# Performance work log

Measured on AMD Instinct MI355X. Metric: run time of the kernel, lower is better.

## Reference

```python
import jax, jax.numpy as jnp
import numpy as np

B, T, P, E = 4, 16, 256, 768
H, D = 12, 64          # num_heads, kq_size; H*D == E
DFF = 3072
SCALE = D ** (-0.5)
EPS = 1e-5


def _ln(x, g, b):
    m = jnp.mean(x, axis=-1, keepdims=True)
    v = jnp.mean((x - m) ** 2, axis=-1, keepdims=True)
    return (x - m) / jnp.sqrt(v + EPS) * g + b


def setup_inputs() -> dict:
    key = jax.random.key(0)
    ks = jax.random.split(key, 16)
    std = 0.02
    d = {"x": jax.random.normal(ks[0], (B, T, P, E), jnp.float32)}
    # spatial attention params (weights stored as (in, out))
    d["sq_w"] = jax.random.normal(ks[1], (E, H * D), jnp.float32) * std
    d["sk_w"] = jax.random.normal(ks[2], (E, H * D), jnp.float32) * std
    d["sv_w"] = jax.random.normal(ks[3], (E, H * D), jnp.float32) * std
    d["so_w"] = jax.random.normal(ks[4], (H * D, E), jnp.float32) * std
    d["sq_b"] = jnp.zeros((H * D,), jnp.float32)
    d["sk_b"] = jnp.zeros((H * D,), jnp.float32)
    d["sv_b"] = jnp.zeros((H * D,), jnp.float32)
    d["so_b"] = jnp.zeros((E,), jnp.float32)
    d["sg"] = jnp.ones((E,), jnp.float32)
    d["sb"] = jnp.zeros((E,), jnp.float32)
    # temporal attention params
    d["tq_w"] = jax.random.normal(ks[5], (E, H * D), jnp.float32) * std
    d["tk_w"] = jax.random.normal(ks[6], (E, H * D), jnp.float32) * std
    d["tv_w"] = jax.random.normal(ks[7], (E, H * D), jnp.float32) * std
    d["to_w"] = jax.random.normal(ks[8], (H * D, E), jnp.float32) * std
    d["tq_b"] = jnp.zeros((H * D,), jnp.float32)
    d["tk_b"] = jnp.zeros((H * D,), jnp.float32)
    d["tv_b"] = jnp.zeros((H * D,), jnp.float32)
    d["to_b"] = jnp.zeros((E,), jnp.float32)
    d["tg"] = jnp.ones((E,), jnp.float32)
    d["tb"] = jnp.zeros((E,), jnp.float32)
    # FFN + final layernorm
    d["w1"] = jax.random.normal(ks[9], (E, DFF), jnp.float32) * std
    d["b1"] = jnp.zeros((DFF,), jnp.float32)
    d["w2"] = jax.random.normal(ks[10], (DFF, E), jnp.float32) * std
    d["b2"] = jnp.zeros((E,), jnp.float32)
    d["g"] = jnp.ones((E,), jnp.float32)
    d["bb"] = jnp.zeros((E,), jnp.float32)
    return d


def reference(x, sq_w, sq_b, sk_w, sk_b, sv_w, sv_b, so_w, so_b, sg, sb,
              tq_w, tq_b, tk_w, tk_b, tv_w, tv_b, to_w, to_b, tg, tb,
              w1, b1, w2, b2, g, bb):
    b, t, p, e = x.shape

    # ---- Spatial layer: attention over patches P within each frame ----
    q = (x @ sq_w + sq_b).reshape(b, t, p, H, D)
    k = (x @ sk_w + sk_b).reshape(b, t, p, H, D)
    v = (x @ sv_w + sv_b).reshape(b, t, p, H, D)
    attn = jnp.einsum('btphd,btqhd->bthpq', q, k) * SCALE
    attn = jax.nn.softmax(attn, axis=-1)
    out = jnp.einsum('bthpq,btqhd->btphd', attn, v).reshape(b, t, p, H * D)
    out = out @ so_w + so_b
    x = _ln(x + out, sg, sb)

    # ---- Temporal layer: causal attention over frames T per patch ----
    q = (x @ tq_w + tq_b).reshape(b, t, p, H, D)
    k = (x @ tk_w + tk_b).reshape(b, t, p, H, D)
    v = (x @ tv_w + tv_b).reshape(b, t, p, H, D)
    attn = jnp.einsum('btphd,bsphd->bphts', q, k) * SCALE
    causal = jnp.where(jnp.arange(t)[:, None] >= jnp.arange(t)[None, :],
                       jnp.float32(0), -jnp.inf).astype(x.dtype)  # (T, T)
    attn = attn + causal
    attn = jax.nn.softmax(attn, axis=-1)
    out = jnp.einsum('bphts,bsphd->btphd', attn, v).reshape(b, t, p, H * D)
    out = out @ to_w + to_b
    x = _ln(x + out, tg, tb)

    # ---- Feed forward + final layernorm ----
    ff = jax.nn.gelu(x @ w1 + b1, approximate=False) @ w2 + b2
    x = _ln(x + ff, g, bb)
    return x
```

## Files before the change

kernel.cpp:

```cpp
#include <hip/hip_runtime.h>
#include <math.h>

constexpr int cB   = 4;
constexpr int cT   = 16;
constexpr int cP   = 256;
constexpr int cE   = 768;
constexpr int cH   = 12;
constexpr int cD   = 64;
constexpr int cDFF = 3072;
constexpr int NTOK = cB * cT * cP;
constexpr float cSCALE = 0.125f;
constexpr float cEPS = 1e-5f;

typedef __attribute__((ext_vector_type(8))) short short8;
typedef __attribute__((ext_vector_type(4))) float f32x4;
typedef __attribute__((ext_vector_type(8))) unsigned short u16x8;
typedef __attribute__((ext_vector_type(4))) unsigned short u16x4;

#define AS1 __attribute__((address_space(1)))
#define AS3 __attribute__((address_space(3)))

__device__ inline float b2f(unsigned short u) {
    union { unsigned int i; float f; } c; c.i = ((unsigned int)u) << 16; return c.f;
}
__device__ inline unsigned short f2b(float f) {
    union { float f; unsigned int i; } c; c.f = f;
    unsigned int i = c.i;
    unsigned int r = i + 0x7FFFu + ((i >> 16) & 1u);
    return (unsigned short)(r >> 16);
}

__device__ inline void gload16(const unsigned short* g, short* l) {
    __builtin_amdgcn_global_load_lds((AS1 const void*)g, (AS3 void*)l, 16, 0, 0);
}

__device__ inline void stage_half(const unsigned short* Xg, int K,
                                  short* ldsbase, int w, int l) {
    #pragma unroll
    for (int j = 0; j < 2; ++j) {
        const int r = w * 16 + j * 8 + (l >> 3);
        const int sl = l & 7;
        gload16(Xg + (size_t)r * K + ((sl ^ (r & 7)) << 3),
                ldsbase + r * 64 + (sl << 3));
    }
}

template<int OUTB, int ACT, int SPLIT3>
__global__ __launch_bounds__(512, 2) void gemm256_kernel(
    const unsigned short* __restrict__ A,
    const unsigned short* __restrict__ BT,
    const float* __restrict__ bias0, const float* __restrict__ bias1,
    const float* __restrict__ bias2,
    void* __restrict__ C0, void* __restrict__ C1, void* __restrict__ C2,
    int M, int N, int K, int nbn)
{
    __shared__ short As[2 * 256 * 64];
    __shared__ short Bs[2 * 256 * 64];

    const int tid = threadIdx.x;
    const int w = tid >> 6, l = tid & 63;
    const int l15 = l & 15, l16 = l >> 4;
    const int wm = w >> 2, wn = w & 3;

    const int nwg = gridDim.x;
    const int wg = (blockIdx.x & 7) * (nwg >> 3) + (blockIdx.x >> 3);
    const int bm = wg / nbn, bn = wg % nbn;
    const int m0 = bm * 256, n0 = bn * 256;

    const unsigned short* pA0 = A + (size_t)m0 * K;
    const unsigned short* pA1 = A + (size_t)(m0 + 128) * K;
    const unsigned short* pB0 = BT + (size_t)n0 * K;
    const unsigned short* pB1 = BT + (size_t)(n0 + 128) * K;

    f32x4 acc[8][4];
    #pragma unroll
    for (int i = 0; i < 8; ++i)
        #pragma unroll
        for (int j = 0; j < 4; ++j)
            #pragma unroll
            for (int r = 0; r < 4; ++r) acc[i][j][r] = 0.f;

    stage_half(pA0, K, As, w, l);
    stage_half(pA1, K, As + 8192, w, l);
    stage_half(pB0, K, Bs, w, l);
    stage_half(pB1, K, Bs + 8192, w, l);
    asm volatile("s_waitcnt vmcnt(0)" ::: "memory");
    __builtin_amdgcn_s_barrier();

    short8 bF[4][2];
    const int niter = K >> 7;
    int k0 = 0;
    for (int it = 0; it < niter; ++it) {
        const int kb = k0 + 64;
        const int kc = (k0 + 128 < K) ? (k0 + 128) : 0;
        #pragma unroll
        for (int p = 0; p < 8; ++p) {
            const int c = p >> 2;
            const int q = p & 3;

            short8 aF[2][2];
            if (q == 0) {
                #pragma unroll
                for (int nf = 0; nf < 4; ++nf) {
                    const int rb = wn * 64 + nf * 16 + l15;
                    const char* pb = (const char*)Bs + c * 32768 + rb * 128;
                    const int sw = (rb & 7) << 4;
                    bF[nf][0] = *(const short8*)(pb + ((l16 * 16) ^ sw));
                    bF[nf][1] = *(const short8*)(pb + ((64 + l16 * 16) ^ sw));
                }
            }
            #pragma unroll
            for (int mm = 0; mm < 2; ++mm) {
                const int ra = wm * 128 + (q * 2 + mm) * 16 + l15;
                const char* pa = (const char*)As + c * 32768 + ra * 128;
                const int sw = (ra & 7) << 4;
                aF[mm][0] = *(const short8*)(pa + ((l16 * 16) ^ sw));
                aF[mm][1] = *(const short8*)(pa + ((64 + l16 * 16) ^ sw));
            }

            {
                const int koff = (p < 4) ? kb : kc;
                short* dst = ((q < 2) ? As : Bs) + ((c ^ 1) * 16384) + ((q & 1) * 8192);
                const unsigned short* src =
                    (q == 0 ? pA0 : q == 1 ? pA1 : q == 2 ? pB0 : pB1) + koff;
                stage_half(src, K, dst, w, l);
            }

            __builtin_amdgcn_s_barrier();
            asm volatile("s_waitcnt lgkmcnt(0)" ::: "memory");
            __builtin_amdgcn_sched_barrier(0);
            __builtin_amdgcn_s_setprio(1);
            #pragma unroll
            for (int kk = 0; kk < 2; ++kk)
                #pragma unroll
                for (int nf = 0; nf < 4; ++nf)
                    #pragma unroll
                    for (int mm = 0; mm < 2; ++mm)
                        acc[q * 2 + mm][nf] = __builtin_amdgcn_mfma_f32_16x16x32_bf16(
                            aF[mm][kk], bF[nf][kk], acc[q * 2 + mm][nf], 0, 0, 0);
            __builtin_amdgcn_s_setprio(0);
            __builtin_amdgcn_sched_barrier(0);
            if (q == 3)
                asm volatile("s_waitcnt vmcnt(0)" ::: "memory");
            __builtin_amdgcn_s_barrier();
        }
        k0 += 128;
    }

    #pragma unroll
    for (int mf = 0; mf < 8; ++mf) {
        #pragma unroll
        for (int nf = 0; nf < 4; ++nf) {
            const int ng = n0 + wn * 64 + nf * 16 + l15;
            int nl = ng;
            const float* bp = bias0;
            void* Cp = C0;
            int Nout = N;
            if (SPLIT3) {
                const int which = ng / 768;
                nl = ng - which * 768;
                bp = (which == 0) ? bias0 : (which == 1) ? bias1 : bias2;
                Cp = (which == 0) ? C0 : (which == 1) ? C1 : C2;
                Nout = 768;
            }
            const float bs = bp[nl];
            #pragma unroll
            for (int r = 0; r < 4; ++r) {
                const int row = m0 + wm * 128 + mf * 16 + l16 * 4 + r;
                float v = acc[mf][nf][r] + bs;
                if (ACT) v = 0.5f * v * (1.f + erff(v * 0.70710678118654752f));
                if (OUTB) ((unsigned short*)Cp)[(size_t)row * Nout + nl] = f2b(v);
                else      ((float*)Cp)[(size_t)row * Nout + nl] = v;
            }
        }
    }
}

__global__ __launch_bounds__(256) void transpose_cast_kernel(
    const float* __restrict__ W, unsigned short* __restrict__ WT,
    int K, int N)
{
    __shared__ float t[32][33];
    const int k0 = blockIdx.y * 32;
    const int n0 = blockIdx.x * 32;
    const int tx = threadIdx.x & 31;
    const int ty4 = (threadIdx.x >> 5) << 2;
    #pragma unroll
    for (int i = 0; i < 4; ++i)
        t[ty4 + i][tx] = W[(size_t)(k0 + ty4 + i) * N + n0 + tx];
    __syncthreads();
    #pragma unroll
    for (int i = 0; i < 4; ++i)
        WT[(size_t)(n0 + ty4 + i) * K + k0 + tx] = f2b(t[tx][ty4 + i]);
}

struct TP8 { const float* src[8]; unsigned short* dst[8]; };
__global__ __launch_bounds__(256) void transpose_cast8_kernel(TP8 p)
{
    __shared__ float t[32][33];
    const int z = blockIdx.z;
    const float* W = p.src[z];
    unsigned short* WT = p.dst[z];
    const int k0 = blockIdx.y * 32;
    const int n0 = blockIdx.x * 32;
    const int tx = threadIdx.x & 31;
    const int ty4 = (threadIdx.x >> 5) << 2;
    #pragma unroll
    for (int i = 0; i < 4; ++i)
        t[ty4 + i][tx] = W[(size_t)(k0 + ty4 + i) * cE + n0 + tx];
    __syncthreads();
    #pragma unroll
    for (int i = 0; i < 4; ++i)
        WT[(size_t)(n0 + ty4 + i) * cE + k0 + tx] = f2b(t[tx][ty4 + i]);
}

__global__ __launch_bounds__(256) void cast_bf16_kernel(
    const float* __restrict__ in, unsigned short* __restrict__ out, int n4)
{
    for (int i = blockIdx.x * blockDim.x + threadIdx.x; i < n4;
         i += gridDim.x * blockDim.x) {
        float4 v = ((const float4*)in)[i];
        u16x4 o;
        o[0] = f2b(v.x); o[1] = f2b(v.y); o[2] = f2b(v.z); o[3] = f2b(v.w);
        *(u16x4*)(out + (size_t)i * 4) = o;
    }
}

__global__ __launch_bounds__(256) void residual_ln_kernel(
    const float* __restrict__ X, const float* __restrict__ R,
    const float* __restrict__ gamma, const float* __restrict__ beta,
    float* __restrict__ out, unsigned short* __restrict__ outb)
{
    const int row = blockIdx.x;
    const size_t off = (size_t)row * cE;
    const int tid = threadIdx.x;

    float v[3];
    float s = 0.f, ss = 0.f;
    #pragma unroll
    for (int i = 0; i < 3; ++i) {
        const int e = tid + i * 256;
        const float t = X[off + e] + R[off + e];
        v[i] = t; s += t; ss += t * t;
    }
    #pragma unroll
    for (int o = 32; o > 0; o >>= 1) {
        s  += __shfl_down(s, o);
        ss += __shfl_down(ss, o);
    }
    __shared__ float rs[4], rss[4];
    const int wid = tid >> 6;
    if ((tid & 63) == 0) { rs[wid] = s; rss[wid] = ss; }
    __syncthreads();
    s  = rs[0] + rs[1] + rs[2] + rs[3];
    ss = rss[0] + rss[1] + rss[2] + rss[3];

    const float mean = s * (1.f / cE);
    const float var  = ss * (1.f / cE) - mean * mean;
    const float inv  = rsqrtf(var + cEPS);
    #pragma unroll
    for (int i = 0; i < 3; ++i) {
        const int e = tid + i * 256;
        const float r = (v[i] - mean) * inv * gamma[e] + beta[e];
        out[off + e] = r;
        if (outb) outb[off + e] = f2b(r);
    }
}

__global__ __launch_bounds__(256) void spatial_attn_mfma_kernel(
    const unsigned short* __restrict__ Q, const unsigned short* __restrict__ K,
    const unsigned short* __restrict__ V, unsigned short* __restrict__ O)
{
    __shared__ short Ks[64 * 64];
    __shared__ short Vt[64 * 64];
    __shared__ short Ps[4][64 * 64];

    const int bid = blockIdx.x;
    const int h  = bid % cH;
    const int bt = bid / cH;
    const size_t base = (size_t)bt * cP * cE + h * cD;

    const int tid = threadIdx.x;
    const int w = tid >> 6, l = tid & 63;
    const int l15 = l & 15, l16 = l >> 4;

    short8 qf[4][2];
    #pragma unroll
    for (int mf = 0; mf < 4; ++mf)
        #pragma unroll
        for (int kf = 0; kf < 2; ++kf)
            qf[mf][kf] = *(const short8*)(
                Q + base + (size_t)(w * 64 + mf * 16 + l15) * cE + kf * 32 + l16 * 8);

    f32x4 o[4][4];
    float mrun[4][4], lrun[4][4];
    #pragma unroll
    for (int mf = 0; mf < 4; ++mf)
        #pragma unroll
        for (int j = 0; j < 4; ++j) {
            #pragma unroll
            for (int r = 0; r < 4; ++r) o[mf][j][r] = 0.f;
            mrun[mf][j] = -INFINITY; lrun[mf][j] = 0.f;
        }

    const int krow = w * 8 + (l >> 3);
    const int kc16 = l & 7;
    const int vj  = tid & 31;
    const int vd0 = (tid >> 5) * 8;

    for (int c0 = 0; c0 < cP; c0 += 64) {
        __syncthreads();
        #pragma unroll
        for (int p = 0; p < 2; ++p) {
            const int row = p * 32 + krow;
            gload16(K + base + (size_t)(c0 + row) * cE + ((kc16 ^ (row & 7)) << 3),
                    Ks + row * 64 + kc16 * 8);
        }
        #pragma unroll
        for (int p = 0; p < 2; ++p) {
            const int j = p * 32 + vj;
            short8 vv = *(const short8*)(V + base + (size_t)(c0 + j) * cE + vd0);
            char* vb = (char*)Vt;
            #pragma unroll
            for (int e = 0; e < 8; ++e) {
                const int row = vd0 + e;
                *(short*)(vb + row * 128 + ((2 * j) ^ ((row & 7) << 4))) = vv[e];
            }
        }
        __syncthreads();

        f32x4 s[4][4];
        #pragma unroll
        for (int mf = 0; mf < 4; ++mf)
            #pragma unroll
            for (int nf = 0; nf < 4; ++nf)
                #pragma unroll
                for (int r = 0; r < 4; ++r) s[mf][nf][r] = 0.f;

        #pragma unroll
        for (int nf = 0; nf < 4; ++nf) {
            const int row = nf * 16 + l15;
            const char* kb = (const char*)Ks + row * 128;
            const int sw = (row & 7) << 4;
            short8 k0 = *(const short8*)(kb + ((l16 * 16) ^ sw));
            short8 k1 = *(const short8*)(kb + ((64 + l16 * 16) ^ sw));
            #pragma unroll
            for (int mf = 0; mf < 4; ++mf) {
                s[mf][nf] = __builtin_amdgcn_mfma_f32_16x16x32_bf16(qf[mf][0], k0, s[mf][nf], 0, 0, 0);
                s[mf][nf] = __builtin_amdgcn_mfma_f32_16x16x32_bf16(qf[mf][1], k1, s[mf][nf], 0, 0, 0);
            }
        }

        #pragma unroll
        for (int mf = 0; mf < 4; ++mf)
            #pragma unroll
            for (int nf = 0; nf < 4; ++nf)
                #pragma unroll
                for (int r = 0; r < 4; ++r) s[mf][nf][r] *= cSCALE;

        #pragma unroll
        for (int mf = 0; mf < 4; ++mf) {
            #pragma unroll
            for (int r = 0; r < 4; ++r) {
                float rv = fmaxf(fmaxf(s[mf][0][r], s[mf][1][r]),
                                 fmaxf(s[mf][2][r], s[mf][3][r]));
                rv = fmaxf(rv, __shfl_xor(rv, 1));
                rv = fmaxf(rv, __shfl_xor(rv, 2));
                rv = fmaxf(rv, __shfl_xor(rv, 4));
                rv = fmaxf(rv, __shfl_xor(rv, 8));
                const float mn = fmaxf(mrun[mf][r], rv);
                const float al = __expf(mrun[mf][r] - mn);
                mrun[mf][r] = mn;
                float ps = 0.f;
                #pragma unroll
                for (int nf = 0; nf < 4; ++nf) {
                    const float pe = __expf(s[mf][nf][r] - mn);
                    s[mf][nf][r] = pe;
                    ps += pe;
                }
                ps += __shfl_xor(ps, 1);
                ps += __shfl_xor(ps, 2);
                ps += __shfl_xor(ps, 4);
                ps += __shfl_xor(ps, 8);
                lrun[mf][r] = lrun[mf][r] * al + ps;
                #pragma unroll
                for (int df = 0; df < 4; ++df) o[mf][df][r] *= al;
            }
        }

        char* pw = (char*)&Ps[w][0];
        #pragma unroll
        for (int mf = 0; mf < 4; ++mf)
            #pragma unroll
            for (int nf = 0; nf < 4; ++nf)
                #pragma unroll
                for (int r = 0; r < 4; ++r) {
                    const int row = mf * 16 + l16 * 4 + r;
                    *(short*)(pw + row * 128 + (((nf * 16 + l15) * 2) ^ ((row & 7) << 4))) =
                        (short)f2b(s[mf][nf][r]);
                }

        short8 pa[4][2];
        #pragma unroll
        for (int mf = 0; mf < 4; ++mf) {
            const int prow = mf * 16 + l15;
            const char* pb = (const char*)&Ps[w][0] + prow * 128;
            const int sw = (prow & 7) << 4;
            pa[mf][0] = *(const short8*)(pb + ((l16 * 16) ^ sw));
            pa[mf][1] = *(const short8*)(pb + ((64 + l16 * 16) ^ sw));
        }
        #pragma unroll
        for (int df = 0; df < 4; ++df) {
            const int vrow = df * 16 + l15;
            const char* vbb = (const char*)Vt + vrow * 128;
            const int sw = (vrow & 7) << 4;
            short8 v0 = *(const short8*)(vbb + ((l16 * 16) ^ sw));
            short8 v1 = *(const short8*)(vbb + ((64 + l16 * 16) ^ sw));
            #pragma unroll
            for (int mf = 0; mf < 4; ++mf) {
                o[mf][df] = __builtin_amdgcn_mfma_f32_16x16x32_bf16(pa[mf][0], v0, o[mf][df], 0, 0, 0);
                o[mf][df] = __builtin_amdgcn_mfma_f32_16x16x32_bf16(pa[mf][1], v1, o[mf][df], 0, 0, 0);
            }
        }
    }

    #pragma unroll
    for (int mf = 0; mf < 4; ++mf)
        #pragma unroll
        for (int r = 0; r < 4; ++r) {
            const float inv = 1.f / lrun[mf][r];
            const size_t rowoff = base + (size_t)(w * 64 + mf * 16 + l16 * 4 + r) * cE;
            #pragma unroll
            for (int df = 0; df < 4; ++df)
                O[rowoff + df * 16 + l15] = f2b(o[mf][df][r] * inv);
        }
}

__global__ __launch_bounds__(128) void temporal_attn_kernel(
    const unsigned short* __restrict__ Q, const unsigned short* __restrict__ Kb,
    const unsigned short* __restrict__ V, unsigned short* __restrict__ O)
{
    const int bid = blockIdx.x;
    const int hg  = bid & 1;
    const int bp  = bid >> 1;
    const int p   = bp % cP;
    const int b   = bp / cP;

    __shared__ float Ks[cT][6][cD + 1];
    __shared__ float Vs[cT][6][cD + 1];

    const size_t framestride = (size_t)cP * cE;
    const size_t base0 = ((size_t)(b * cT) * cP + p) * cE + hg * 384;

    for (int li = threadIdx.x; li < cT * 384; li += 128) {
        const int s = li / 384;
        const int r = li % 384;
        const size_t src = base0 + (size_t)s * framestride + r;
        Ks[s][r / 64][r & 63] = b2f(Kb[src]);
        Vs[s][r / 64][r & 63] = b2f(V[src]);
    }
    __syncthreads();
    if (threadIdx.x >= 96) return;

    const int hh = threadIdx.x >> 4;
    const int t  = threadIdx.x & 15;
    const size_t qoff = ((size_t)(b * cT + t) * cP + p) * cE + hg * 384 + hh * cD;

    float q[cD];
    #pragma unroll
    for (int d = 0; d < cD; d += 8) {
        short8 f = *(const short8*)(Q + qoff + d);
        #pragma unroll
        for (int j = 0; j < 8; ++j) q[d + j] = b2f((unsigned short)f[j]);
    }

    float sc[cT];
    float mx = -INFINITY;
    #pragma unroll
    for (int s = 0; s < cT; ++s) {
        float acc = 0.f;
        #pragma unroll
        for (int d = 0; d < cD; ++d) acc = fmaf(q[d], Ks[s][hh][d], acc);
        sc[s] = (s <= t) ? acc * cSCALE : -INFINITY;
        mx = fmaxf(mx, sc[s]);
    }
    float l = 0.f;
    #pragma unroll
    for (int s = 0; s < cT; ++s) {
        const float e_ = __expf(sc[s] - mx);
        sc[s] = e_;
        l += e_;
    }
    float o[cD];
    #pragma unroll
    for (int d = 0; d < cD; ++d) o[d] = 0.f;
    #pragma unroll
    for (int s = 0; s < cT; ++s) {
        const float pj = sc[s];
        #pragma unroll
        for (int d = 0; d < cD; ++d) o[d] = fmaf(pj, Vs[s][hh][d], o[d]);
    }
    const float invl = 1.f / l;
    unsigned short* op = O + qoff;
    #pragma unroll
    for (int d = 0; d < cD; d += 8) {
        u16x8 f;
        #pragma unroll
        for (int j = 0; j < 8; ++j) f[j] = f2b(o[d + j] * invl);
        *(u16x8*)(op + d) = f;
    }
}

extern "C" void kernel_launch(void* const* d_in, const int* in_sizes, int n_in,
                              void* d_out, int out_size, void* d_ws, size_t ws_size,
                              hipStream_t stream)
{
    const float* x    = (const float*)d_in[0];
    const float* sq_w = (const float*)d_in[1];
    const float* sk_w = (const float*)d_in[2];
    const float* sv_w = (const float*)d_in[3];
    const float* so_w = (const float*)d_in[4];
    const float* sq_b = (const float*)d_in[5];
    const float* sk_b = (const float*)d_in[6];
    const float* sv_b = (const float*)d_in[7];
    const float* so_b = (const float*)d_in[8];
    const float* sg   = (const float*)d_in[9];
    const float* sb   = (const float*)d_in[10];
    const float* tq_w = (const float*)d_in[11];
    const float* tk_w = (const float*)d_in[12];
    const float* tv_w = (const float*)d_in[13];
    const float* to_w = (const float*)d_in[14];
    const float* tq_b = (const float*)d_in[15];
    const float* tk_b = (const float*)d_in[16];
    const float* tv_b = (const float*)d_in[17];
    const float* to_b = (const float*)d_in[18];
    const float* tg   = (const float*)d_in[19];
    const float* tb   = (const float*)d_in[20];
    const float* w1   = (const float*)d_in[21];
    const float* b1   = (const float*)d_in[22];
    const float* w2   = (const float*)d_in[23];
    const float* b2   = (const float*)d_in[24];
    const float* g    = (const float*)d_in[25];
    const float* bb   = (const float*)d_in[26];

    const size_t NE = (size_t)NTOK * cE;
    const size_t EE = (size_t)cE * cE;

    float* W0 = (float*)d_ws;
    float* Wp = W0 + NE;
    unsigned short* Xb = (unsigned short*)(Wp + NE);
    unsigned short* Qb = Xb + NE;
    unsigned short* Kbuf = Qb + NE;
    unsigned short* Vb = Kbuf + NE;
    unsigned short* Ob = Vb + NE;
    unsigned short* Hb = Qb;
    unsigned short* WT = Ob + NE;
    unsigned short* sqT = WT;
    unsigned short* skT = sqT + EE;
    unsigned short* svT = skT + EE;
    unsigned short* soT = svT + EE;
    unsigned short* tqT = soT + EE;
    unsigned short* tkT = tqT + EE;
    unsigned short* tvT = tkT + EE;
    unsigned short* toT = tvT + EE;
    unsigned short* w1T = toT + EE;
    unsigned short* w2T = w1T + (size_t)cDFF * cE;

    const dim3 blk(256);
    const dim3 blk512(512);
    const dim3 gLN(NTOK);
    const dim3 gQKV(576);
    const dim3 gOUT(192);
    const dim3 gFF1(768);

    cast_bf16_kernel<<<dim3(2048), blk, 0, stream>>>(x, Xb, (int)(NE / 4));
    {
        TP8 p;
        p.src[0] = sq_w; p.dst[0] = sqT;
        p.src[1] = sk_w; p.dst[1] = skT;
        p.src[2] = sv_w; p.dst[2] = svT;
        p.src[3] = so_w; p.dst[3] = soT;
        p.src[4] = tq_w; p.dst[4] = tqT;
        p.src[5] = tk_w; p.dst[5] = tkT;
        p.src[6] = tv_w; p.dst[6] = tvT;
        p.src[7] = to_w; p.dst[7] = toT;
        transpose_cast8_kernel<<<dim3(cE / 32, cE / 32, 8), blk, 0, stream>>>(p);
    }
    transpose_cast_kernel<<<dim3(cDFF / 32, cE / 32), blk, 0, stream>>>(w1, w1T, cE, cDFF);
    transpose_cast_kernel<<<dim3(cE / 32, cDFF / 32), blk, 0, stream>>>(w2, w2T, cDFF, cE);

    gemm256_kernel<1,0,1><<<gQKV, blk512, 0, stream>>>(
        Xb, sqT, sq_b, sk_b, sv_b, Qb, Kbuf, Vb, NTOK, 2304, cE, 9);
    spatial_attn_mfma_kernel<<<dim3(cB * cT * cH), blk, 0, stream>>>(Qb, Kbuf, Vb, Ob);
    gemm256_kernel<0,0,0><<<gOUT, blk512, 0, stream>>>(
        Ob, soT, so_b, nullptr, nullptr, Wp, nullptr, nullptr, NTOK, cE, cE, 3);
    residual_ln_kernel<<<gLN, blk, 0, stream>>>(x, Wp, sg, sb, W0, Xb);

    gemm256_kernel<1,0,1><<<gQKV, blk512, 0, stream>>>(
        Xb, tqT, tq_b, tk_b, tv_b, Qb, Kbuf, Vb, NTOK, 2304, cE, 9);
    temporal_attn_kernel<<<dim3(cB * cP * 2), dim3(128), 0, stream>>>(Qb, Kbuf, Vb, Ob);
    gemm256_kernel<0,0,0><<<gOUT, blk512, 0, stream>>>(
        Ob, toT, to_b, nullptr, nullptr, Wp, nullptr, nullptr, NTOK, cE, cE, 3);
    residual_ln_kernel<<<gLN, blk, 0, stream>>>(W0, Wp, tg, tb, W0, Xb);

    gemm256_kernel<1,1,0><<<gFF1, blk512, 0, stream>>>(
        Xb, w1T, b1, nullptr, nullptr, Hb, nullptr, nullptr, NTOK, cDFF, cE, 12);
    gemm256_kernel<0,0,0><<<gOUT, blk512, 0, stream>>>(
        Hb, w2T, b2, nullptr, nullptr, Wp, nullptr, nullptr, NTOK, cE, cDFF, 3);
    residual_ln_kernel<<<gLN, blk, 0, stream>>>(W0, Wp, g, bb, (float*)d_out, nullptr);
}
```

Before: 755.5 us.

## Switch GEMM to 256x128 tiles with triple-buffered LDS pipeline

Rewrites the bf16 MFMA GEMM to use 256x128 output tiles with a 4x2 wave layout instead of 256x256 with 2x4. The old ping-pong scheme with eight barriers per 128-K step becomes a three-stage LDS ring over 64-wide K slices, prefetched two stages ahead with partial vmcnt/lgkmcnt waits. Grids are doubled so each GEMM launches twice as many workgroups. This aims to cut barrier overhead, raise occupancy/parallelism on the many CUs, and overlap loads with MFMA, at the cost of lower per-tile data reuse (more global traffic for A) and 96KB of LDS per block.

```diff
diff --git a/kernel.cpp b/kernel.cpp
--- a/kernel.cpp
+++ b/kernel.cpp
@@ -34,17 +34,6 @@
     __builtin_amdgcn_global_load_lds((AS1 const void*)g, (AS3 void*)l, 16, 0, 0);
 }
 
-__device__ inline void stage_half(const unsigned short* Xg, int K,
-                                  short* ldsbase, int w, int l) {
-    #pragma unroll
-    for (int j = 0; j < 2; ++j) {
-        const int r = w * 16 + j * 8 + (l >> 3);
-        const int sl = l & 7;
-        gload16(Xg + (size_t)r * K + ((sl ^ (r & 7)) << 3),
-                ldsbase + r * 64 + (sl << 3));
-    }
-}
-
 template<int OUTB, int ACT, int SPLIT3>
 __global__ __launch_bounds__(512, 2) void gemm256_kernel(
     const unsigned short* __restrict__ A,
@@ -54,101 +43,133 @@
     void* __restrict__ C0, void* __restrict__ C1, void* __restrict__ C2,
     int M, int N, int K, int nbn)
 {
-    __shared__ short As[2 * 256 * 64];
-    __shared__ short Bs[2 * 256 * 64];
+    __shared__ short LDS[3 * 24576];
 
     const int tid = threadIdx.x;
     const int w = tid >> 6, l = tid & 63;
     const int l15 = l & 15, l16 = l >> 4;
-    const int wm = w >> 2, wn = w & 3;
+    const int wm = w >> 1, wn = w & 1;
+    const int srow = l >> 3;
+    const int sslot = l & 7;
 
     const int nwg = gridDim.x;
     const int wg = (blockIdx.x & 7) * (nwg >> 3) + (blockIdx.x >> 3);
     const int bm = wg / nbn, bn = wg % nbn;
-    const int m0 = bm * 256, n0 = bn * 256;
-
-    const unsigned short* pA0 = A + (size_t)m0 * K;
-    const unsigned short* pA1 = A + (size_t)(m0 + 128) * K;
-    const unsigned short* pB0 = BT + (size_t)n0 * K;
-    const unsigned short* pB1 = BT + (size_t)(n0 + 128) * K;
-
-    f32x4 acc[8][4];
-    #pragma unroll
-    for (int i = 0; i < 8; ++i)
+    const int m0 = bm * 256, n0 = bn * 128;
+
+    const unsigned short* pA = A + (size_t)m0 * K;
+    const unsigned short* pB = BT + (size_t)n0 * K;
+
+    f32x4 acc[4][4];
+    #pragma unroll
+    for (int i = 0; i < 4; ++i)
         #pragma unroll
         for (int j = 0; j < 4; ++j)
             #pragma unroll
             for (int r = 0; r < 4; ++r) acc[i][j][r] = 0.f;
 
-    stage_half(pA0, K, As, w, l);
-    stage_half(pA1, K, As + 8192, w, l);
-    stage_half(pB0, K, Bs, w, l);
-    stage_half(pB1, K, Bs + 8192, w, l);
-    asm volatile("s_waitcnt vmcnt(0)" ::: "memory");
+    const int nt = K >> 6;
+
+    #define STAGE_A(t_, buf_)                                                   \
+        {                                                                       \
+            const unsigned short* src_ = pA + (t_) * 64;                        \
+            short* dst_ = LDS + (buf_) * 24576;                                 \
+            _Pragma("unroll")                                                   \
+            for (int j_ = 0; j_ < 4; ++j_) {                                    \
+                const int r_ = w * 32 + j_ * 8 + srow;                          \
+                gload16(src_ + (size_t)r_ * K + ((sslot ^ (r_ & 7)) << 3),      \
+                        dst_ + r_ * 64 + (sslot << 3));                         \
+            }                                                                   \
+        }
+    #define STAGE_B(t_, buf_)                                                   \
+        {                                                                       \
+            const unsigned short* src_ = pB + (t_) * 64;                        \
+            short* dst_ = LDS + (buf_) * 24576 + 16384;                         \
+            _Pragma("unroll")                                                   \
+            for (int j_ = 0; j_ < 2; ++j_) {                                    \
+                const int r_ = w * 8 + j_ * 64 + srow;                          \
+                gload16(src_ + (size_t)r_ * K + ((sslot ^ (r_ & 7)) << 3),      \
+                        dst_ + r_ * 64 + (sslot << 3));                         \
+            }                                                                   \
+        }
+
+    STAGE_A(0, 0); STAGE_B(0, 0);
+    STAGE_A(1, 1); STAGE_B(1, 1);
+    asm volatile("s_waitcnt vmcnt(6)" ::: "memory");
     __builtin_amdgcn_s_barrier();
 
-    short8 bF[4][2];
-    const int niter = K >> 7;
-    int k0 = 0;
-    for (int it = 0; it < niter; ++it) {
-        const int kb = k0 + 64;
-        const int kc = (k0 + 128 < K) ? (k0 + 128) : 0;
-        #pragma unroll
-        for (int p = 0; p < 8; ++p) {
-            const int c = p >> 2;
-            const int q = p & 3;
-
-            short8 aF[2][2];
-            if (q == 0) {
-                #pragma unroll
-                for (int nf = 0; nf < 4; ++nf) {
-                    const int rb = wn * 64 + nf * 16 + l15;
-                    const char* pb = (const char*)Bs + c * 32768 + rb * 128;
-                    const int sw = (rb & 7) << 4;
-                    bF[nf][0] = *(const short8*)(pb + ((l16 * 16) ^ sw));
-                    bF[nf][1] = *(const short8*)(pb + ((64 + l16 * 16) ^ sw));
-                }
-            }
-            #pragma unroll
-            for (int mm = 0; mm < 2; ++mm) {
-                const int ra = wm * 128 + (q * 2 + mm) * 16 + l15;
-                const char* pa = (const char*)As + c * 32768 + ra * 128;
-                const int sw = (ra & 7) << 4;
-                aF[mm][0] = *(const short8*)(pa + ((l16 * 16) ^ sw));
-                aF[mm][1] = *(const short8*)(pa + ((64 + l16 * 16) ^ sw));
-            }
-
-            {
-                const int koff = (p < 4) ? kb : kc;
-                short* dst = ((q < 2) ? As : Bs) + ((c ^ 1) * 16384) + ((q & 1) * 8192);
-                const unsigned short* src =
-                    (q == 0 ? pA0 : q == 1 ? pA1 : q == 2 ? pB0 : pB1) + koff;
-                stage_half(src, K, dst, w, l);
-            }
-
-            __builtin_amdgcn_s_barrier();
-            asm volatile("s_waitcnt lgkmcnt(0)" ::: "memory");
-            __builtin_amdgcn_sched_barrier(0);
-            __builtin_amdgcn_s_setprio(1);
-            #pragma unroll
-            for (int kk = 0; kk < 2; ++kk)
-                #pragma unroll
-                for (int nf = 0; nf < 4; ++nf)
-                    #pragma unroll
-                    for (int mm = 0; mm < 2; ++mm)
-                        acc[q * 2 + mm][nf] = __builtin_amdgcn_mfma_f32_16x16x32_bf16(
-                            aF[mm][kk], bF[nf][kk], acc[q * 2 + mm][nf], 0, 0, 0);
-            __builtin_amdgcn_s_setprio(0);
-            __builtin_amdgcn_sched_barrier(0);
-            if (q == 3)
+    int buf = 0;
+    for (int t = 0; t < nt; ++t) {
+        const short* bA = LDS + buf * 24576;
+        const short* bB = bA + 16384;
+
+        short8 aF[4][2], bF[4][2];
+        #pragma unroll
+        for (int mm = 0; mm < 4; ++mm) {
+            const int ra = wm * 64 + mm * 16 + l15;
+            const char* pa = (const char*)bA + ra * 128;
+            aF[mm][0] = *(const short8*)(pa + ((l16 * 16) ^ ((ra & 7) << 4)));
+        }
+        #pragma unroll
+        for (int nf = 0; nf < 4; ++nf) {
+            const int rb = wn * 64 + nf * 16 + l15;
+            const char* pb = (const char*)bB + rb * 128;
+            bF[nf][0] = *(const short8*)(pb + ((l16 * 16) ^ ((rb & 7) << 4)));
+        }
+        __builtin_amdgcn_sched_barrier(0);
+        #pragma unroll
+        for (int mm = 0; mm < 4; ++mm) {
+            const int ra = wm * 64 + mm * 16 + l15;
+            const char* pa = (const char*)bA + ra * 128;
+            aF[mm][1] = *(const short8*)(pa + ((64 + l16 * 16) ^ ((ra & 7) << 4)));
+        }
+        #pragma unroll
+        for (int nf = 0; nf < 4; ++nf) {
+            const int rb = wn * 64 + nf * 16 + l15;
+            const char* pb = (const char*)bB + rb * 128;
+            bF[nf][1] = *(const short8*)(pb + ((64 + l16 * 16) ^ ((rb & 7) << 4)));
+        }
+
+        if (t + 2 < nt) {
+            const int b2 = (buf == 0) ? 2 : buf - 1;
+            STAGE_A(t + 2, b2); STAGE_B(t + 2, b2);
+        }
+
+        asm volatile("s_waitcnt lgkmcnt(8)" ::: "memory");
+        __builtin_amdgcn_sched_barrier(0);
+        __builtin_amdgcn_s_setprio(1);
+        #pragma unroll
+        for (int nf = 0; nf < 4; ++nf)
+            #pragma unroll
+            for (int mm = 0; mm < 4; ++mm)
+                acc[mm][nf] = __builtin_amdgcn_mfma_f32_16x16x32_bf16(
+                    aF[mm][0], bF[nf][0], acc[mm][nf], 0, 0, 0);
+        __builtin_amdgcn_s_setprio(0);
+        asm volatile("s_waitcnt lgkmcnt(0)" ::: "memory");
+        __builtin_amdgcn_sched_barrier(0);
+        __builtin_amdgcn_s_setprio(1);
+        #pragma unroll
+        for (int nf = 0; nf < 4; ++nf)
+            #pragma unroll
+            for (int mm = 0; mm < 4; ++mm)
+                acc[mm][nf] = __builtin_amdgcn_mfma_f32_16x16x32_bf16(
+                    aF[mm][1], bF[nf][1], acc[mm][nf], 0, 0, 0);
+        __builtin_amdgcn_s_setprio(0);
+
+        if (t + 1 < nt) {
+            if (t + 2 < nt)
+                asm volatile("s_waitcnt vmcnt(6)" ::: "memory");
+            else
                 asm volatile("s_waitcnt vmcnt(0)" ::: "memory");
             __builtin_amdgcn_s_barrier();
         }
-        k0 += 128;
-    }
-
-    #pragma unroll
-    for (int mf = 0; mf < 8; ++mf) {
+        buf = (buf == 2) ? 0 : buf + 1;
+    }
+    #undef STAGE_A
+    #undef STAGE_B
+
+    #pragma unroll
+    for (int mf = 0; mf < 4; ++mf) {
         #pragma unroll
         for (int nf = 0; nf < 4; ++nf) {
             const int ng = n0 + wn * 64 + nf * 16 + l15;
@@ -166,7 +187,7 @@
             const float bs = bp[nl];
             #pragma unroll
             for (int r = 0; r < 4; ++r) {
-                const int row = m0 + wm * 128 + mf * 16 + l16 * 4 + r;
+                const int row = m0 + wm * 64 + mf * 16 + l16 * 4 + r;
                 float v = acc[mf][nf][r] + bs;
                 if (ACT) v = 0.5f * v * (1.f + erff(v * 0.70710678118654752f));
                 if (OUTB) ((unsigned short*)Cp)[(size_t)row * Nout + nl] = f2b(v);
@@ -569,9 +590,9 @@
     const dim3 blk(256);
     const dim3 blk512(512);
     const dim3 gLN(NTOK);
-    const dim3 gQKV(576);
-    const dim3 gOUT(192);
-    const dim3 gFF1(768);
+    const dim3 gQKV(1152);
+    const dim3 gOUT(384);
+    const dim3 gFF1(1536);
 
     cast_bf16_kernel<<<dim3(2048), blk, 0, stream>>>(x, Xb, (int)(NE / 4));
     {
@@ -590,22 +611,22 @@
     transpose_cast_kernel<<<dim3(cE / 32, cDFF / 32), blk, 0, stream>>>(w2, w2T, cDFF, cE);
 
     gemm256_kernel<1,0,1><<<gQKV, blk512, 0, stream>>>(
-        Xb, sqT, sq_b, sk_b, sv_b, Qb, Kbuf, Vb, NTOK, 2304, cE, 9);
+        Xb, sqT, sq_b, sk_b, sv_b, Qb, Kbuf, Vb, NTOK, 2304, cE, 18);
     spatial_attn_mfma_kernel<<<dim3(cB * cT * cH), blk, 0, stream>>>(Qb, Kbuf, Vb, Ob);
     gemm256_kernel<0,0,0><<<gOUT, blk512, 0, stream>>>(
-        Ob, soT, so_b, nullptr, nullptr, Wp, nullptr, nullptr, NTOK, cE, cE, 3);
+        Ob, soT, so_b, nullptr, nullptr, Wp, nullptr, nullptr, NTOK, cE, cE, 6);
     residual_ln_kernel<<<gLN, blk, 0, stream>>>(x, Wp, sg, sb, W0, Xb);
 
     gemm256_kernel<1,0,1><<<gQKV, blk512, 0, stream>>>(
-        Xb, tqT, tq_b, tk_b, tv_b, Qb, Kbuf, Vb, NTOK, 2304, cE, 9);
+        Xb, tqT, tq_b, tk_b, tv_b, Qb, Kbuf, Vb, NTOK, 2304, cE, 18);
     temporal_attn_kernel<<<dim3(cB * cP * 2), dim3(128), 0, stream>>>(Qb, Kbuf, Vb, Ob);
     gemm256_kernel<0,0,0><<<gOUT, blk512, 0, stream>>>(
-        Ob, toT, to_b, nullptr, nullptr, Wp, nullptr, nullptr, NTOK, cE, cE, 3);
+        Ob, toT, to_b, nullptr, nullptr, Wp, nullptr, nullptr, NTOK, cE, cE, 6);
     residual_ln_kernel<<<gLN, blk, 0, stream>>>(W0, Wp, tg, tb, W0, Xb);
 
     gemm256_kernel<1,1,0><<<gFF1, blk512, 0, stream>>>(
-        Xb, w1T, b1, nullptr, nullptr, Hb, nullptr, nullptr, NTOK, cDFF, cE, 12);
+        Xb, w1T, b1, nullptr, nullptr, Hb, nullptr, nullptr, NTOK, cDFF, cE, 24);
     gemm256_kernel<0,0,0><<<gOUT, blk512, 0, stream>>>(
-        Hb, w2T, b2, nullptr, nullptr, Wp, nullptr, nullptr, NTOK, cE, cDFF, 3);
+        Hb, w2T, b2, nullptr, nullptr, Wp, nullptr, nullptr, NTOK, cE, cDFF, 6);
     residual_ln_kernel<<<gLN, blk, 0, stream>>>(W0, Wp, g, bb, (float*)d_out, nullptr);
 }
```

Result: faster. 710.8 us (-5.9%).
